# Kernel optimization log

Hardware: AMD Instinct MI355X
Metric: run time of the kernel (lower is better)

The kernel has to match this reference:

```python
import jax, jax.numpy as jnp
import numpy as np

TOP_K = 2
SCALING = 32.0 / 64.0  # lora_alpha / reservoir_size


def setup_inputs() -> dict:
    key = jax.random.key(0)
    ks = jax.random.split(key, 6)
    Bsz, S, Din, Dout, R, E = 4, 2048, 4096, 4096, 64, 16
    x = jax.random.normal(ks[0], (Bsz, S, Din), dtype=jnp.float32)
    base_w = jax.random.normal(ks[1], (Dout, Din), dtype=jnp.float32) * 0.02
    base_b = jax.random.normal(ks[2], (Dout,), dtype=jnp.float32) * 0.02
    A = jax.random.normal(ks[3], (R, Din), dtype=jnp.float32) * (1.0 / np.sqrt(Din))
    B = jax.random.normal(ks[4], (E, Dout, R), dtype=jnp.float32) * 0.02
    router_w = jax.random.normal(ks[5], (E, Din), dtype=jnp.float32) * 0.02
    return {"x": x, "base_w": base_w, "base_b": base_b, "A": A, "B": B, "router_w": router_w}


def reference(x, base_w, base_b, A, B, router_w):
    # base linear: [b,s,din] @ [dout,din]^T + bias
    base_out = jnp.einsum('bsi,oi->bso', x, base_w) + base_b
    # low-rank projection through fixed reservoir A (activation=identity, dropout off)
    res_hidden = jnp.einsum('bsi,ri->bsr', x, A)          # [b,s,r]
    # routing
    logits = jnp.einsum('bsi,ei->bse', x, router_w)       # [b,s,E]
    probs = jax.nn.softmax(logits, axis=-1)
    topw, topi = jax.lax.top_k(probs, TOP_K)              # [b,s,k]
    topw = topw / (jnp.sum(topw, axis=-1, keepdims=True) + 1e-6)
    num_experts = B.shape[0]
    # combine weights per expert: sum_k w_k * onehot(idx_k)  -> [b,s,E]
    combine = jnp.sum(jax.nn.one_hot(topi, num_experts, dtype=x.dtype) * topw[..., None], axis=-2)
    # weighted per-expert lowrank B matmul and combine
    delta = jnp.einsum('bse,bsr,eor->bso', combine, res_hidden, B)
    return base_out + delta * SCALING
```

## Files before the change

### kernel.cpp

```cpp
#include <hip/hip_runtime.h>
#include <cstdint>
#include <cstddef>

typedef short short8 __attribute__((ext_vector_type(8)));
typedef float f32x4 __attribute__((ext_vector_type(4)));

#define DIN  4096
#define DOUT 4096
#define RANK 64
#define NEXP 16
#define NTOK 8192
#define KCAT 5120

__device__ __forceinline__ unsigned short f2bf(float f) {
    unsigned int u = __builtin_bit_cast(unsigned int, f);
    u = (u + 0x7FFFu + ((u >> 16) & 1u)) >> 16;
    return (unsigned short)u;
}
__device__ __forceinline__ float bf2f(unsigned short h) {
    unsigned int u = ((unsigned int)h) << 16;
    return __builtin_bit_cast(float, u);
}
__device__ __forceinline__ void async_cp16(const void* g, void* lds) {
    __builtin_amdgcn_global_load_lds(
        (const __attribute__((address_space(1))) void*)g,
        (__attribute__((address_space(3))) void*)lds, 16, 0, 0);
}

__global__ void __launch_bounds__(256) prep_w_kernel(
        const float* __restrict__ bw, const float* __restrict__ Bm,
        const float* __restrict__ Am, const float* __restrict__ rw,
        unsigned short* __restrict__ Wcat, unsigned short* __restrict__ W1) {
    const unsigned NG1 = (unsigned)DOUT * KCAT / 8u;
    const unsigned NGT = NG1 + 96u * DIN / 8u;
    for (unsigned g = blockIdx.x * blockDim.x + threadIdx.x; g < NGT;
         g += gridDim.x * blockDim.x) {
        const float* src;
        unsigned short* dst;
        int mode = 0;
        if (g < NG1) {
            unsigned o  = g / 640u;
            unsigned c8 = (g - o * 640u) * 8u;
            dst = Wcat + (size_t)o * KCAT + c8;
            if (c8 < DIN) {
                src = bw + (size_t)o * DIN + c8;
            } else {
                unsigned cc = c8 - DIN;
                unsigned e = cc >> 6, r = cc & 63u;
                src = Bm + ((size_t)e * DOUT + o) * RANK + r;
            }
        } else {
            unsigned g2 = g - NG1;
            unsigned row = g2 / 512u;
            unsigned c8  = (g2 - row * 512u) * 8u;
            dst = W1 + (size_t)row * DIN + c8;
            if (row < 64u)       src = Am + (size_t)row * DIN + c8;
            else if (row < 80u)  src = rw + (size_t)(row - 64u) * DIN + c8;
            else               { src = rw + (size_t)(row - 80u) * DIN + c8; mode = 1; }
        }
        float4 v0 = *(const float4*)(src);
        float4 v1 = *(const float4*)(src + 4);
        float vv[8] = {v0.x, v0.y, v0.z, v0.w, v1.x, v1.y, v1.z, v1.w};
        unsigned short o16[8];
        #pragma unroll
        for (int i = 0; i < 8; ++i) {
            unsigned short h = f2bf(vv[i]);
            if (mode) h = f2bf(vv[i] - bf2f(h));
            o16[i] = h;
        }
        uint4 pk;
        pk.x = (unsigned)o16[0] | ((unsigned)o16[1] << 16);
        pk.y = (unsigned)o16[2] | ((unsigned)o16[3] << 16);
        pk.z = (unsigned)o16[4] | ((unsigned)o16[5] << 16);
        pk.w = (unsigned)o16[6] | ((unsigned)o16[7] << 16);
        *(uint4*)dst = pk;
    }
}

__global__ void __launch_bounds__(256) prep_x_kernel(
        const float* __restrict__ x, const float* __restrict__ rw,
        unsigned short* __restrict__ Xcat, float* __restrict__ Corr,
        float* __restrict__ Z) {
    __shared__ __align__(16) float xsl[8][532];
    __shared__ __align__(16) float red[8][16][16];
    const int tid = threadIdx.x;

    {
        unsigned gtid = blockIdx.x * 256u + tid;
        if (gtid < (unsigned)(NTOK * 96 / 4)) {
            f32x4 z = {0.f, 0.f, 0.f, 0.f};
            ((f32x4*)Z)[gtid] = z;
        }
    }
    const int t0 = blockIdx.x * 8;
    const int tt = tid >> 5, l32 = tid & 31;
    const int eg = tid >> 6, ts = (tid >> 4) & 3, cc = tid & 15;
    float part[2][4] = {};

    for (int w = 0; w < 8; ++w) {
        #pragma unroll
        for (int sub = 0; sub < 4; ++sub) {
            const int col = w * 512 + sub * 128 + l32 * 4;
            const float4 xv = *(const float4*)&x[(size_t)(t0 + tt) * DIN + col];
            unsigned short b0 = f2bf(xv.x), b1 = f2bf(xv.y),
                           b2 = f2bf(xv.z), b3 = f2bf(xv.w);
            uint2 pk = { (unsigned)b0 | ((unsigned)b1 << 16),
                         (unsigned)b2 | ((unsigned)b3 << 16) };
            *(uint2*)&Xcat[(size_t)(t0 + tt) * KCAT + col] = pk;
            float4 xl = { xv.x - bf2f(b0), xv.y - bf2f(b1),
                          xv.z - bf2f(b2), xv.w - bf2f(b3) };
            *(float4*)&xsl[tt][sub * 128 + l32 * 4] = xl;
        }
        __syncthreads();
        #pragma unroll
        for (int j = 0; j < 8; ++j) {
            const int colb = w * 512 + (j * 16 + cc) * 4;
            const float4 r0 = *(const float4*)&rw[(size_t)(eg * 4 + 0) * DIN + colb];
            const float4 r1 = *(const float4*)&rw[(size_t)(eg * 4 + 1) * DIN + colb];
            const float4 r2 = *(const float4*)&rw[(size_t)(eg * 4 + 2) * DIN + colb];
            const float4 r3 = *(const float4*)&rw[(size_t)(eg * 4 + 3) * DIN + colb];
            #pragma unroll
            for (int t2 = 0; t2 < 2; ++t2) {
                const int t = ts * 2 + t2;
                const float4 xv = *(const float4*)&xsl[t][(j * 16 + cc) * 4];
                part[t2][0] += xv.x * r0.x + xv.y * r0.y + xv.z * r0.z + xv.w * r0.w;
                part[t2][1] += xv.x * r1.x + xv.y * r1.y + xv.z * r1.z + xv.w * r1.w;
                part[t2][2] += xv.x * r2.x + xv.y * r2.y + xv.z * r2.z + xv.w * r2.w;
                part[t2][3] += xv.x * r3.x + xv.y * r3.y + xv.z * r3.z + xv.w * r3.w;
            }
        }
        __syncthreads();
    }
    #pragma unroll
    for (int t2 = 0; t2 < 2; ++t2)
        #pragma unroll
        for (int e = 0; e < 4; ++e)
            red[ts * 2 + t2][eg * 4 + e][cc] = part[t2][e];
    __syncthreads();
    if (tid < 128) {
        const int t = tid >> 4, e = tid & 15;
        float s = 0.f;
        #pragma unroll
        for (int c = 0; c < 16; ++c) s += red[t][e][c];
        Corr[(size_t)(t0 + t) * NEXP + e] = s;
    }
}

__global__ void __launch_bounds__(256) gemm_prep_kernel(
        const unsigned short* __restrict__ Xcat,
        const unsigned short* __restrict__ W1, float* __restrict__ Z) {
    __shared__ __align__(16) unsigned short Xs[128 * 64];
    __shared__ __align__(16) unsigned short Ws[96 * 64];
    const int tid = threadIdx.x;
    const int wave = tid >> 6, lane = tid & 63;
    const int quad = lane >> 4, l16 = lane & 15;
    const int bm0 = blockIdx.x * 128;
    const int ks0 = blockIdx.y * 512;
    const int srow = tid >> 3;
    const int scol = ((tid & 7) ^ (srow & 7)) * 8;
    const int wm = wave * 32;
    f32x4 acc[2][6] = {};
    for (int kt = 0; kt < 8; ++kt) {
        const int k0 = ks0 + kt * 64;
        #pragma unroll
        for (int i = 0; i < 4; ++i)
            async_cp16(Xcat + (size_t)(bm0 + i * 32 + srow) * KCAT + k0 + scol,
                       (char*)Xs + i * 4096 + wave * 1024);
        #pragma unroll
        for (int i = 0; i < 3; ++i)
            async_cp16(W1 + (size_t)(i * 32 + srow) * DIN + k0 + scol,
                       (char*)Ws + i * 4096 + wave * 1024);
        __syncthreads();
        #pragma unroll
        for (int kk = 0; kk < 2; ++kk) {
            short8 am[2], bn[6];
            #pragma unroll
            for (int i = 0; i < 2; ++i)
                am[i] = *(const short8*)&Xs[(wm + i * 16 + l16) * 64 +
                                            (((kk * 4 + quad) ^ (l16 & 7)) << 3)];
            #pragma unroll
            for (int j = 0; j < 6; ++j)
                bn[j] = *(const short8*)&Ws[(j * 16 + l16) * 64 +
                                            (((kk * 4 + quad) ^ (l16 & 7)) << 3)];
            #pragma unroll
            for (int i = 0; i < 2; ++i)
                #pragma unroll
                for (int j = 0; j < 6; ++j)
                    acc[i][j] = __builtin_amdgcn_mfma_f32_16x16x32_bf16(
                        am[i], bn[j], acc[i][j], 0, 0, 0);
        }
        __syncthreads();
    }
    #pragma unroll
    for (int i = 0; i < 2; ++i) {
        const int row0 = bm0 + wm + i * 16 + quad * 4;
        #pragma unroll
        for (int j = 0; j < 6; ++j) {
            const int col = j * 16 + l16;
            #pragma unroll
            for (int r = 0; r < 4; ++r)
                atomicAdd(&Z[(size_t)(row0 + r) * 96 + col], acc[i][j][r]);
        }
    }
}

__global__ void __launch_bounds__(256) finalize_kernel(
        const float* __restrict__ Z, const float* __restrict__ Corr,
        unsigned short* __restrict__ Xcat) {
    __shared__ __align__(16) unsigned short hb[4][1024];
    const int tid = threadIdx.x, wv = tid >> 6, lane = tid & 63;
    const int t = blockIdx.x * 4 + wv;
    const float h = Z[(size_t)t * 96 + lane];
    float l[16];
    #pragma unroll
    for (int e = 0; e < 16; ++e)
        l[e] = Z[(size_t)t * 96 + 64 + e] + Z[(size_t)t * 96 + 80 + e]
             + Corr[(size_t)t * NEXP + e];
    int i1 = 0; float b1v = l[0];
    #pragma unroll
    for (int e = 1; e < 16; ++e) if (l[e] > b1v) { b1v = l[e]; i1 = e; }
    int i2 = -1; float b2v = -1e30f;
    #pragma unroll
    for (int e = 0; e < 16; ++e) if (e != i1 && l[e] > b2v) { b2v = l[e]; i2 = e; }
    float S = 0.f;
    #pragma unroll
    for (int e = 0; e < 16; ++e) S += expf(l[e] - b1v);
    const float t1 = 1.0f / S;
    const float t2 = expf(b2v - b1v) / S;
    const float d = t1 + t2 + 1e-6f;
    const float c1 = 0.5f * t1 / d;
    const float c2 = 0.5f * t2 / d;
    #pragma unroll
    for (int e = 0; e < 16; ++e) {
        const float v = (e == i1) ? c1 * h : (e == i2) ? c2 * h : 0.0f;
        hb[wv][e * 64 + lane] = f2bf(v);
    }
    __syncthreads();
    uint4* dst = (uint4*)(Xcat + (size_t)t * KCAT + DIN);
    const uint4* src = (const uint4*)hb[wv];
    dst[lane * 2] = src[lane * 2];
    dst[lane * 2 + 1] = src[lane * 2 + 1];
}

__global__ void __launch_bounds__(256) gemm_main_kernel(
        const unsigned short* __restrict__ Xcat,
        const unsigned short* __restrict__ Wcat,
        const float* __restrict__ bias, float* __restrict__ out) {
    __shared__ __align__(16) unsigned short Xs[128 * 64];
    __shared__ __align__(16) unsigned short Ws[128 * 64];
    const int tid = threadIdx.x;
    const int wave = tid >> 6, lane = tid & 63;
    const int quad = lane >> 4, l16 = lane & 15;
    const int bn0 = blockIdx.x * 128;
    const int bm0 = blockIdx.y * 128;
    const int srow = tid >> 3;
    const int scol = ((tid & 7) ^ (srow & 7)) * 8;
    const unsigned short* gx = Xcat + (size_t)(bm0 + srow) * KCAT + scol;
    const unsigned short* gw = Wcat + (size_t)(bn0 + srow) * KCAT + scol;
    const int wm0 = (wave & 1) * 64;
    const int wn0 = (wave >> 1) * 64;
    f32x4 acc[4][4] = {};
    for (int kt = 0; kt < KCAT / 64; ++kt) {
        const int k0 = kt * 64;
        #pragma unroll
        for (int i = 0; i < 4; ++i) {
            async_cp16(gx + (size_t)(i * 32) * KCAT + k0, (char*)Xs + i * 4096 + wave * 1024);
            async_cp16(gw + (size_t)(i * 32) * KCAT + k0, (char*)Ws + i * 4096 + wave * 1024);
        }
        __syncthreads();
        #pragma unroll
        for (int kk = 0; kk < 2; ++kk) {
            short8 am[4], bn[4];
            #pragma unroll
            for (int i = 0; i < 4; ++i)
                am[i] = *(const short8*)&Xs[(wm0 + i * 16 + l16) * 64 +
                                            (((kk * 4 + quad) ^ (l16 & 7)) << 3)];
            #pragma unroll
            for (int j = 0; j < 4; ++j)
                bn[j] = *(const short8*)&Ws[(wn0 + j * 16 + l16) * 64 +
                                            (((kk * 4 + quad) ^ (l16 & 7)) << 3)];
            #pragma unroll
            for (int i = 0; i < 4; ++i)
                #pragma unroll
                for (int j = 0; j < 4; ++j)
                    acc[i][j] = __builtin_amdgcn_mfma_f32_16x16x32_bf16(
                        am[i], bn[j], acc[i][j], 0, 0, 0);
        }
        __syncthreads();
    }
    #pragma unroll
    for (int j = 0; j < 4; ++j) {
        const int col = bn0 + wn0 + j * 16 + l16;
        const float bj = bias[col];
        #pragma unroll
        for (int i = 0; i < 4; ++i) {
            const int row0 = bm0 + wm0 + i * 16 + quad * 4;
            #pragma unroll
            for (int r = 0; r < 4; ++r)
                out[(size_t)(row0 + r) * DOUT + col] = acc[i][j][r] + bj;
        }
    }
}

extern "C" void kernel_launch(void* const* d_in, const int* in_sizes, int n_in,
                              void* d_out, int out_size, void* d_ws, size_t ws_size,
                              hipStream_t stream) {
    const float* x  = (const float*)d_in[0];
    const float* bw = (const float*)d_in[1];
    const float* bb = (const float*)d_in[2];
    const float* Am = (const float*)d_in[3];
    const float* Bm = (const float*)d_in[4];
    const float* rw = (const float*)d_in[5];
    float* out = (float*)d_out;
    char* ws = (char*)d_ws;
    unsigned short* Xcat = (unsigned short*)(ws);
    unsigned short* Wcat = (unsigned short*)(ws + 83886080);
    unsigned short* W1   = (unsigned short*)(ws + 125829120);
    float* Z    = (float*)(ws + 126615552);
    float* Corr = (float*)(ws + 129761280);

    hipLaunchKernelGGL(prep_w_kernel,   dim3(4096),   dim3(256), 0, stream, bw, Bm, Am, rw, Wcat, W1);
    hipLaunchKernelGGL(prep_x_kernel,   dim3(1024),   dim3(256), 0, stream, x, rw, Xcat, Corr, Z);
    hipLaunchKernelGGL(gemm_prep_kernel,dim3(64, 8),  dim3(256), 0, stream, Xcat, W1, Z);
    hipLaunchKernelGGL(finalize_kernel, dim3(2048),   dim3(256), 0, stream, Z, Corr, Xcat);
    hipLaunchKernelGGL(gemm_main_kernel,dim3(32, 64), dim3(256), 0, stream, Xcat, Wcat, bb, out);
}
```

Baseline: 742.9 us.

## Fuse prep kernels and compute router logits in fp32 with fused gating projection

Merges weight conversion and x preprocessing into one launch, computing router logits directly in fp32 instead of a bf16 GEMM plus low-order correction. The reservoir projection now runs per 32-token block over full K without split-K atomics or Z zeroing, and applies top-2 gating in its epilogue, removing the separate finalize kernel. This cuts launches and intermediate traffic but gives the projection kernel only 256 blocks with a long serial K loop.

```diff
diff --git a/kernel.cpp b/kernel.cpp
--- a/kernel.cpp
+++ b/kernel.cpp
@@ -17,229 +17,196 @@
     u = (u + 0x7FFFu + ((u >> 16) & 1u)) >> 16;
     return (unsigned short)u;
 }
-__device__ __forceinline__ float bf2f(unsigned short h) {
-    unsigned int u = ((unsigned int)h) << 16;
-    return __builtin_bit_cast(float, u);
-}
 __device__ __forceinline__ void async_cp16(const void* g, void* lds) {
     __builtin_amdgcn_global_load_lds(
         (const __attribute__((address_space(1))) void*)g,
         (__attribute__((address_space(3))) void*)lds, 16, 0, 0);
 }
 
-__global__ void __launch_bounds__(256) prep_w_kernel(
+__global__ void __launch_bounds__(256) prep_all_kernel(
+        const float* __restrict__ x, const float* __restrict__ rw,
         const float* __restrict__ bw, const float* __restrict__ Bm,
-        const float* __restrict__ Am, const float* __restrict__ rw,
-        unsigned short* __restrict__ Wcat, unsigned short* __restrict__ W1) {
-    const unsigned NG1 = (unsigned)DOUT * KCAT / 8u;
-    const unsigned NGT = NG1 + 96u * DIN / 8u;
-    for (unsigned g = blockIdx.x * blockDim.x + threadIdx.x; g < NGT;
-         g += gridDim.x * blockDim.x) {
-        const float* src;
-        unsigned short* dst;
-        int mode = 0;
-        if (g < NG1) {
-            unsigned o  = g / 640u;
-            unsigned c8 = (g - o * 640u) * 8u;
-            dst = Wcat + (size_t)o * KCAT + c8;
-            if (c8 < DIN) {
-                src = bw + (size_t)o * DIN + c8;
-            } else {
-                unsigned cc = c8 - DIN;
-                unsigned e = cc >> 6, r = cc & 63u;
-                src = Bm + ((size_t)e * DOUT + o) * RANK + r;
-            }
-        } else {
-            unsigned g2 = g - NG1;
-            unsigned row = g2 / 512u;
-            unsigned c8  = (g2 - row * 512u) * 8u;
-            dst = W1 + (size_t)row * DIN + c8;
-            if (row < 64u)       src = Am + (size_t)row * DIN + c8;
-            else if (row < 80u)  src = rw + (size_t)(row - 64u) * DIN + c8;
-            else               { src = rw + (size_t)(row - 80u) * DIN + c8; mode = 1; }
-        }
-        float4 v0 = *(const float4*)(src);
-        float4 v1 = *(const float4*)(src + 4);
-        float vv[8] = {v0.x, v0.y, v0.z, v0.w, v1.x, v1.y, v1.z, v1.w};
-        unsigned short o16[8];
-        #pragma unroll
-        for (int i = 0; i < 8; ++i) {
-            unsigned short h = f2bf(vv[i]);
-            if (mode) h = f2bf(vv[i] - bf2f(h));
-            o16[i] = h;
-        }
-        uint4 pk;
-        pk.x = (unsigned)o16[0] | ((unsigned)o16[1] << 16);
-        pk.y = (unsigned)o16[2] | ((unsigned)o16[3] << 16);
-        pk.z = (unsigned)o16[4] | ((unsigned)o16[5] << 16);
-        pk.w = (unsigned)o16[6] | ((unsigned)o16[7] << 16);
-        *(uint4*)dst = pk;
-    }
-}
-
-__global__ void __launch_bounds__(256) prep_x_kernel(
-        const float* __restrict__ x, const float* __restrict__ rw,
-        unsigned short* __restrict__ Xcat, float* __restrict__ Corr,
-        float* __restrict__ Z) {
+        const float* __restrict__ Am,
+        unsigned short* __restrict__ Xcat, unsigned short* __restrict__ Wcat,
+        unsigned short* __restrict__ W1A, float* __restrict__ Lg) {
     __shared__ __align__(16) float xsl[8][532];
     __shared__ __align__(16) float red[8][16][16];
     const int tid = threadIdx.x;
 
-    {
-        unsigned gtid = blockIdx.x * 256u + tid;
-        if (gtid < (unsigned)(NTOK * 96 / 4)) {
-            f32x4 z = {0.f, 0.f, 0.f, 0.f};
-            ((f32x4*)Z)[gtid] = z;
-        }
-    }
-    const int t0 = blockIdx.x * 8;
-    const int tt = tid >> 5, l32 = tid & 31;
-    const int eg = tid >> 6, ts = (tid >> 4) & 3, cc = tid & 15;
-    float part[2][4] = {};
-
-    for (int w = 0; w < 8; ++w) {
-        #pragma unroll
-        for (int sub = 0; sub < 4; ++sub) {
-            const int col = w * 512 + sub * 128 + l32 * 4;
-            const float4 xv = *(const float4*)&x[(size_t)(t0 + tt) * DIN + col];
-            unsigned short b0 = f2bf(xv.x), b1 = f2bf(xv.y),
-                           b2 = f2bf(xv.z), b3 = f2bf(xv.w);
-            uint2 pk = { (unsigned)b0 | ((unsigned)b1 << 16),
-                         (unsigned)b2 | ((unsigned)b3 << 16) };
-            *(uint2*)&Xcat[(size_t)(t0 + tt) * KCAT + col] = pk;
-            float4 xl = { xv.x - bf2f(b0), xv.y - bf2f(b1),
-                          xv.z - bf2f(b2), xv.w - bf2f(b3) };
-            *(float4*)&xsl[tt][sub * 128 + l32 * 4] = xl;
-        }
-        __syncthreads();
-        #pragma unroll
-        for (int j = 0; j < 8; ++j) {
-            const int colb = w * 512 + (j * 16 + cc) * 4;
-            const float4 r0 = *(const float4*)&rw[(size_t)(eg * 4 + 0) * DIN + colb];
-            const float4 r1 = *(const float4*)&rw[(size_t)(eg * 4 + 1) * DIN + colb];
-            const float4 r2 = *(const float4*)&rw[(size_t)(eg * 4 + 2) * DIN + colb];
-            const float4 r3 = *(const float4*)&rw[(size_t)(eg * 4 + 3) * DIN + colb];
-            #pragma unroll
-            for (int t2 = 0; t2 < 2; ++t2) {
-                const int t = ts * 2 + t2;
-                const float4 xv = *(const float4*)&xsl[t][(j * 16 + cc) * 4];
-                part[t2][0] += xv.x * r0.x + xv.y * r0.y + xv.z * r0.z + xv.w * r0.w;
-                part[t2][1] += xv.x * r1.x + xv.y * r1.y + xv.z * r1.z + xv.w * r1.w;
-                part[t2][2] += xv.x * r2.x + xv.y * r2.y + xv.z * r2.z + xv.w * r2.w;
-                part[t2][3] += xv.x * r3.x + xv.y * r3.y + xv.z * r3.z + xv.w * r3.w;
-            }
-        }
-        __syncthreads();
-    }
-    #pragma unroll
-    for (int t2 = 0; t2 < 2; ++t2)
-        #pragma unroll
-        for (int e = 0; e < 4; ++e)
-            red[ts * 2 + t2][eg * 4 + e][cc] = part[t2][e];
-    __syncthreads();
-    if (tid < 128) {
-        const int t = tid >> 4, e = tid & 15;
-        float s = 0.f;
-        #pragma unroll
-        for (int c = 0; c < 16; ++c) s += red[t][e][c];
-        Corr[(size_t)(t0 + t) * NEXP + e] = s;
-    }
-}
-
-__global__ void __launch_bounds__(256) gemm_prep_kernel(
+    if (blockIdx.x < 1024) {
+        const int t0 = blockIdx.x * 8;
+        const int tt = tid >> 5, l32 = tid & 31;
+        const int eg = tid >> 6, ts = (tid >> 4) & 3, cc = tid & 15;
+        float part[2][4] = {};
+
+        for (int w = 0; w < 8; ++w) {
+            #pragma unroll
+            for (int sub = 0; sub < 4; ++sub) {
+                const int col = w * 512 + sub * 128 + l32 * 4;
+                const float4 xv = *(const float4*)&x[(size_t)(t0 + tt) * DIN + col];
+                unsigned short b0 = f2bf(xv.x), b1 = f2bf(xv.y),
+                               b2 = f2bf(xv.z), b3 = f2bf(xv.w);
+                uint2 pk = { (unsigned)b0 | ((unsigned)b1 << 16),
+                             (unsigned)b2 | ((unsigned)b3 << 16) };
+                *(uint2*)&Xcat[(size_t)(t0 + tt) * KCAT + col] = pk;
+                *(float4*)&xsl[tt][sub * 128 + l32 * 4] = xv;
+            }
+            __syncthreads();
+            #pragma unroll
+            for (int j = 0; j < 8; ++j) {
+                const int colb = w * 512 + (j * 16 + cc) * 4;
+                const float4 r0 = *(const float4*)&rw[(size_t)(eg * 4 + 0) * DIN + colb];
+                const float4 r1 = *(const float4*)&rw[(size_t)(eg * 4 + 1) * DIN + colb];
+                const float4 r2 = *(const float4*)&rw[(size_t)(eg * 4 + 2) * DIN + colb];
+                const float4 r3 = *(const float4*)&rw[(size_t)(eg * 4 + 3) * DIN + colb];
+                #pragma unroll
+                for (int t2 = 0; t2 < 2; ++t2) {
+                    const int t = ts * 2 + t2;
+                    const float4 xv = *(const float4*)&xsl[t][(j * 16 + cc) * 4];
+                    part[t2][0] += xv.x * r0.x + xv.y * r0.y + xv.z * r0.z + xv.w * r0.w;
+                    part[t2][1] += xv.x * r1.x + xv.y * r1.y + xv.z * r1.z + xv.w * r1.w;
+                    part[t2][2] += xv.x * r2.x + xv.y * r2.y + xv.z * r2.z + xv.w * r2.w;
+                    part[t2][3] += xv.x * r3.x + xv.y * r3.y + xv.z * r3.z + xv.w * r3.w;
+                }
+            }
+            __syncthreads();
+        }
+        #pragma unroll
+        for (int t2 = 0; t2 < 2; ++t2)
+            #pragma unroll
+            for (int e = 0; e < 4; ++e)
+                red[ts * 2 + t2][eg * 4 + e][cc] = part[t2][e];
+        __syncthreads();
+        if (tid < 128) {
+            const int t = tid >> 4, e = tid & 15;
+            float s = 0.f;
+            #pragma unroll
+            for (int c = 0; c < 16; ++c) s += red[t][e][c];
+            Lg[(size_t)(t0 + t) * NEXP + e] = s;
+        }
+    } else {
+        const unsigned NG1 = (unsigned)DOUT * KCAT / 8u;
+        const unsigned NGT = NG1 + 64u * DIN / 8u;
+        for (unsigned g = (blockIdx.x - 1024) * 256u + tid; g < NGT;
+             g += 2048u * 256u) {
+            const float* src;
+            unsigned short* dst;
+            if (g < NG1) {
+                unsigned o  = g / 640u;
+                unsigned c8 = (g - o * 640u) * 8u;
+                dst = Wcat + (size_t)o * KCAT + c8;
+                if (c8 < DIN) {
+                    src = bw + (size_t)o * DIN + c8;
+                } else {
+                    unsigned cc2 = c8 - DIN;
+                    unsigned e = cc2 >> 6, r = cc2 & 63u;
+                    src = Bm + ((size_t)e * DOUT + o) * RANK + r;
+                }
+            } else {
+                unsigned g2 = g - NG1;
+                unsigned row = g2 >> 9;
+                unsigned c8  = (g2 & 511u) * 8u;
+                dst = W1A + (size_t)row * DIN + c8;
+                src = Am + (size_t)row * DIN + c8;
+            }
+            float4 v0 = *(const float4*)(src);
+            float4 v1 = *(const float4*)(src + 4);
+            uint4 pk;
+            pk.x = (unsigned)f2bf(v0.x) | ((unsigned)f2bf(v0.y) << 16);
+            pk.y = (unsigned)f2bf(v0.z) | ((unsigned)f2bf(v0.w) << 16);
+            pk.z = (unsigned)f2bf(v1.x) | ((unsigned)f2bf(v1.y) << 16);
+            pk.w = (unsigned)f2bf(v1.z) | ((unsigned)f2bf(v1.w) << 16);
+            *(uint4*)dst = pk;
+        }
+    }
+}
+
+__global__ void __launch_bounds__(256) proj_moe_kernel(
         const unsigned short* __restrict__ Xcat,
-        const unsigned short* __restrict__ W1, float* __restrict__ Z) {
-    __shared__ __align__(16) unsigned short Xs[128 * 64];
-    __shared__ __align__(16) unsigned short Ws[96 * 64];
+        const unsigned short* __restrict__ W1A,
+        const float* __restrict__ Lg, unsigned short* __restrict__ XcatW) {
+    __shared__ __align__(16) unsigned short Xs[32 * 64];
+    __shared__ __align__(16) unsigned short Ws[64 * 64];
+    __shared__ __align__(16) float cw[32][16];
+    __shared__ __align__(16) float hbuf[32][68];
     const int tid = threadIdx.x;
     const int wave = tid >> 6, lane = tid & 63;
     const int quad = lane >> 4, l16 = lane & 15;
-    const int bm0 = blockIdx.x * 128;
-    const int ks0 = blockIdx.y * 512;
+    const int t0 = blockIdx.x * 32;
     const int srow = tid >> 3;
     const int scol = ((tid & 7) ^ (srow & 7)) * 8;
-    const int wm = wave * 32;
-    f32x4 acc[2][6] = {};
-    for (int kt = 0; kt < 8; ++kt) {
-        const int k0 = ks0 + kt * 64;
-        #pragma unroll
-        for (int i = 0; i < 4; ++i)
-            async_cp16(Xcat + (size_t)(bm0 + i * 32 + srow) * KCAT + k0 + scol,
-                       (char*)Xs + i * 4096 + wave * 1024);
-        #pragma unroll
-        for (int i = 0; i < 3; ++i)
-            async_cp16(W1 + (size_t)(i * 32 + srow) * DIN + k0 + scol,
+
+    if (tid < 32) {
+        float l[16];
+        #pragma unroll
+        for (int e = 0; e < 16; ++e) l[e] = Lg[(size_t)(t0 + tid) * NEXP + e];
+        int i1 = 0; float b1v = l[0];
+        #pragma unroll
+        for (int e = 1; e < 16; ++e) if (l[e] > b1v) { b1v = l[e]; i1 = e; }
+        int i2 = -1; float b2v = -1e30f;
+        #pragma unroll
+        for (int e = 0; e < 16; ++e) if (e != i1 && l[e] > b2v) { b2v = l[e]; i2 = e; }
+        float S = 0.f;
+        #pragma unroll
+        for (int e = 0; e < 16; ++e) S += expf(l[e] - b1v);
+        const float p1 = 1.0f / S;
+        const float p2 = expf(b2v - b1v) / S;
+        const float d = p1 + p2 + 1e-6f;
+        const float c1 = 0.5f * p1 / d;
+        const float c2 = 0.5f * p2 / d;
+        #pragma unroll
+        for (int e = 0; e < 16; ++e)
+            cw[tid][e] = (e == i1) ? c1 : (e == i2) ? c2 : 0.0f;
+    }
+
+    f32x4 acc[2] = {};
+    for (int kt = 0; kt < DIN / 64; ++kt) {
+        const int k0 = kt * 64;
+        async_cp16(Xcat + (size_t)(t0 + srow) * KCAT + k0 + scol,
+                   (char*)Xs + wave * 1024);
+        #pragma unroll
+        for (int i = 0; i < 2; ++i)
+            async_cp16(W1A + (size_t)(i * 32 + srow) * DIN + k0 + scol,
                        (char*)Ws + i * 4096 + wave * 1024);
         __syncthreads();
         #pragma unroll
         for (int kk = 0; kk < 2; ++kk) {
-            short8 am[2], bn[6];
-            #pragma unroll
-            for (int i = 0; i < 2; ++i)
-                am[i] = *(const short8*)&Xs[(wm + i * 16 + l16) * 64 +
-                                            (((kk * 4 + quad) ^ (l16 & 7)) << 3)];
-            #pragma unroll
-            for (int j = 0; j < 6; ++j)
-                bn[j] = *(const short8*)&Ws[(j * 16 + l16) * 64 +
-                                            (((kk * 4 + quad) ^ (l16 & 7)) << 3)];
-            #pragma unroll
-            for (int i = 0; i < 2; ++i)
-                #pragma unroll
-                for (int j = 0; j < 6; ++j)
-                    acc[i][j] = __builtin_amdgcn_mfma_f32_16x16x32_bf16(
-                        am[i], bn[j], acc[i][j], 0, 0, 0);
+            const int cs = ((kk * 4 + quad) ^ (l16 & 7)) << 3;
+            short8 bn = *(const short8*)&Ws[(wave * 16 + l16) * 64 + cs];
+            #pragma unroll
+            for (int i = 0; i < 2; ++i) {
+                short8 am = *(const short8*)&Xs[(i * 16 + l16) * 64 + cs];
+                acc[i] = __builtin_amdgcn_mfma_f32_16x16x32_bf16(am, bn, acc[i], 0, 0, 0);
+            }
         }
         __syncthreads();
     }
     #pragma unroll
-    for (int i = 0; i < 2; ++i) {
-        const int row0 = bm0 + wm + i * 16 + quad * 4;
-        #pragma unroll
-        for (int j = 0; j < 6; ++j) {
-            const int col = j * 16 + l16;
-            #pragma unroll
-            for (int r = 0; r < 4; ++r)
-                atomicAdd(&Z[(size_t)(row0 + r) * 96 + col], acc[i][j][r]);
-        }
-    }
-}
-
-__global__ void __launch_bounds__(256) finalize_kernel(
-        const float* __restrict__ Z, const float* __restrict__ Corr,
-        unsigned short* __restrict__ Xcat) {
-    __shared__ __align__(16) unsigned short hb[4][1024];
-    const int tid = threadIdx.x, wv = tid >> 6, lane = tid & 63;
-    const int t = blockIdx.x * 4 + wv;
-    const float h = Z[(size_t)t * 96 + lane];
-    float l[16];
+    for (int i = 0; i < 2; ++i)
+        #pragma unroll
+        for (int r = 0; r < 4; ++r)
+            hbuf[i * 16 + quad * 4 + r][wave * 16 + l16] = acc[i][r];
+    __syncthreads();
+    const int t = tid >> 3, part = tid & 7;
+    unsigned short* dst = XcatW + (size_t)(t0 + t) * KCAT + DIN;
     #pragma unroll
-    for (int e = 0; e < 16; ++e)
-        l[e] = Z[(size_t)t * 96 + 64 + e] + Z[(size_t)t * 96 + 80 + e]
-             + Corr[(size_t)t * NEXP + e];
-    int i1 = 0; float b1v = l[0];
-    #pragma unroll
-    for (int e = 1; e < 16; ++e) if (l[e] > b1v) { b1v = l[e]; i1 = e; }
-    int i2 = -1; float b2v = -1e30f;
-    #pragma unroll
-    for (int e = 0; e < 16; ++e) if (e != i1 && l[e] > b2v) { b2v = l[e]; i2 = e; }
-    float S = 0.f;
-    #pragma unroll
-    for (int e = 0; e < 16; ++e) S += expf(l[e] - b1v);
-    const float t1 = 1.0f / S;
-    const float t2 = expf(b2v - b1v) / S;
-    const float d = t1 + t2 + 1e-6f;
-    const float c1 = 0.5f * t1 / d;
-    const float c2 = 0.5f * t2 / d;
-    #pragma unroll
-    for (int e = 0; e < 16; ++e) {
-        const float v = (e == i1) ? c1 * h : (e == i2) ? c2 * h : 0.0f;
-        hb[wv][e * 64 + lane] = f2bf(v);
-    }
-    __syncthreads();
-    uint4* dst = (uint4*)(Xcat + (size_t)t * KCAT + DIN);
-    const uint4* src = (const uint4*)hb[wv];
-    dst[lane * 2] = src[lane * 2];
-    dst[lane * 2 + 1] = src[lane * 2 + 1];
+    for (int ee = 0; ee < 2; ++ee) {
+        const int e = part * 2 + ee;
+        const float c = cw[t][e];
+        #pragma unroll
+        for (int r8 = 0; r8 < 8; ++r8) {
+            uint4 pk;
+            unsigned short o16[8];
+            #pragma unroll
+            for (int k = 0; k < 8; ++k)
+                o16[k] = f2bf(c * hbuf[t][r8 * 8 + k]);
+            pk.x = (unsigned)o16[0] | ((unsigned)o16[1] << 16);
+            pk.y = (unsigned)o16[2] | ((unsigned)o16[3] << 16);
+            pk.z = (unsigned)o16[4] | ((unsigned)o16[5] << 16);
+            pk.w = (unsigned)o16[6] | ((unsigned)o16[7] << 16);
+            *(uint4*)(dst + e * 64 + r8 * 8) = pk;
+        }
+    }
 }
 
 __global__ void __launch_bounds__(256) gemm_main_kernel(
@@ -315,13 +282,13 @@
     char* ws = (char*)d_ws;
     unsigned short* Xcat = (unsigned short*)(ws);
     unsigned short* Wcat = (unsigned short*)(ws + 83886080);
-    unsigned short* W1   = (unsigned short*)(ws + 125829120);
-    float* Z    = (float*)(ws + 126615552);
-    float* Corr = (float*)(ws + 129761280);
-
-    hipLaunchKernelGGL(prep_w_kernel,   dim3(4096),   dim3(256), 0, stream, bw, Bm, Am, rw, Wcat, W1);
-    hipLaunchKernelGGL(prep_x_kernel,   dim3(1024),   dim3(256), 0, stream, x, rw, Xcat, Corr, Z);
-    hipLaunchKernelGGL(gemm_prep_kernel,dim3(64, 8),  dim3(256), 0, stream, Xcat, W1, Z);
-    hipLaunchKernelGGL(finalize_kernel, dim3(2048),   dim3(256), 0, stream, Z, Corr, Xcat);
-    hipLaunchKernelGGL(gemm_main_kernel,dim3(32, 64), dim3(256), 0, stream, Xcat, Wcat, bb, out);
-}
+    unsigned short* W1A  = (unsigned short*)(ws + 125829120);
+    float* Lg = (float*)(ws + 126353408);
+
+    hipLaunchKernelGGL(prep_all_kernel, dim3(3072),   dim3(256), 0, stream,
+                       x, rw, bw, Bm, Am, Xcat, Wcat, W1A, Lg);
+    hipLaunchKernelGGL(proj_moe_kernel, dim3(256),    dim3(256), 0, stream,
+                       Xcat, W1A, Lg, Xcat);
+    hipLaunchKernelGGL(gemm_main_kernel, dim3(32, 64), dim3(256), 0, stream,
+                       Xcat, Wcat, bb, out);
+}
```

After: 750.1 us. Within noise of the previous version (+1.0%).
